# Optimization experiments

Hardware: AMD Instinct MI355X
Metric: run time of the kernel (lower is better)

Reference implementation:

```python
import jax, jax.numpy as jnp
import numpy as np

NG, NP = 4096, 512
ALPHA, BETA = 0.1, 0.5
NON_NEGATIVITY = True


def setup_inputs() -> dict:
    key = jax.random.key(0)
    k1, k2, k3, k4, k5 = jax.random.split(key, 5)
    B, T = 64, 100
    v = jax.random.normal(k1, (B, T, 2), dtype=jnp.float32)
    p0 = jax.random.normal(k2, (B, NP), dtype=jnp.float32)
    # xavier_uniform: limit = sqrt(6/(fan_in+fan_out))
    def xavier(k, shape):
        fan_out, fan_in = shape
        lim = float(np.sqrt(6.0 / (fan_in + fan_out)))
        return jax.random.uniform(k, shape, jnp.float32, -lim, lim)
    W_enc = xavier(k3, (NG, NP))   # init_position_encoder weight
    W_in = xavier(k4, (NG, 2))     # RNN weight_ih_l0
    W_h = xavier(k5, (NG, NG))     # RNN weight_hh_l0
    k6 = jax.random.fold_in(key, 6)
    W_dec = xavier(k6, (NP, NG))   # decoder weight
    return {"v": v, "p0": p0, "W_enc": W_enc, "W_in": W_in, "W_h": W_h, "W_dec": W_dec}


def _rnn(v, h0, W_in, W_h):
    # v: [B,T,2], h0: [B,Ng]
    def step(carry, v_t):
        hidden, vv, z_prev = carry
        z = v_t @ W_in.T + hidden @ W_h.T - BETA * vv  # [B,Ng]
        vv = vv + ALPHA * (z_prev - vv)
        if NON_NEGATIVITY:
            vv = jax.nn.relu(vv)
        s_z = jax.nn.relu(z)
        return (s_z, vv, z), s_z
    zeros = jnp.zeros_like(h0)
    _, out = jax.lax.scan(step, (h0, zeros, zeros), jnp.swapaxes(v, 0, 1))
    return jnp.swapaxes(out, 0, 1)  # [B,T,Ng]


def reference(v, p0, W_enc, W_in, W_h, W_dec):
    h0 = p0 @ W_enc.T                 # [B,Ng]
    gs = _rnn(v, h0, W_in, W_h)       # [B,T,Ng]
    logits = gs @ W_dec.T             # [B,T,Np]
    return jax.nn.log_softmax(logits, axis=-1)
```

## Files before the change

### kernel.cpp

```cpp
#include <hip/hip_runtime.h>
#include <hip/hip_bf16.h>

#define T_STEPS 100
#define NG 4096
#define NP 512

typedef __bf16 bf16x8 __attribute__((ext_vector_type(8)));
typedef float f32x4 __attribute__((ext_vector_type(4)));

__device__ __forceinline__ f32x4 mfma_bf16(bf16x8 a, bf16x8 b, f32x4 c) {
  return __builtin_amdgcn_mfma_f32_16x16x32_bf16(a, b, c, 0, 0, 0);
}

__device__ __forceinline__ void gload16(const void* g, void* l) {
  __builtin_amdgcn_global_load_lds(
      (const __attribute__((address_space(1))) void*)g,
      (__attribute__((address_space(3))) void*)l, 16, 0, 0);
}

__global__ __launch_bounds__(256) void cvt_bf16_kernel(const float* __restrict__ in,
                                                       __hip_bfloat16* __restrict__ out,
                                                       int n8) {
  int i = blockIdx.x * 256 + threadIdx.x;
  if (i >= n8) return;
  const float4* p = reinterpret_cast<const float4*>(in) + (size_t)i * 2;
  float4 f0 = p[0], f1 = p[1];
  union { __hip_bfloat16 h[8]; uint4 u; } z;
  z.h[0] = __float2bfloat16(f0.x); z.h[1] = __float2bfloat16(f0.y);
  z.h[2] = __float2bfloat16(f0.z); z.h[3] = __float2bfloat16(f0.w);
  z.h[4] = __float2bfloat16(f1.x); z.h[5] = __float2bfloat16(f1.y);
  z.h[6] = __float2bfloat16(f1.z); z.h[7] = __float2bfloat16(f1.w);
  *(reinterpret_cast<uint4*>(out) + i) = z.u;
}

__global__ __launch_bounds__(256) void encoder_kernel(const float* __restrict__ p0,
                                                      const float* __restrict__ Wenc,
                                                      __hip_bfloat16* __restrict__ h0) {
  __shared__ float sp[64 * 129];
  const int tid = threadIdx.x;
  const int nb = blockIdx.x * 16;
  const int b = tid & 63;
  const int jg = tid >> 6;
  float acc[4] = {0.f, 0.f, 0.f, 0.f};
  for (int kc = 0; kc < NP; kc += 128) {
    __syncthreads();
    #pragma unroll
    for (int i = 0; i < 32; ++i) {
      int e = tid + i * 256;
      int bb = e >> 7, kk = e & 127;
      sp[bb * 129 + kk] = p0[bb * NP + kc + kk];
    }
    __syncthreads();
    for (int kk = 0; kk < 128; ++kk) {
      float pv = sp[b * 129 + kk];
      #pragma unroll
      for (int jj = 0; jj < 4; ++jj)
        acc[jj] += pv * Wenc[(size_t)(nb + jg * 4 + jj) * NP + kc + kk];
    }
  }
  #pragma unroll
  for (int jj = 0; jj < 4; ++jj)
    h0[(size_t)b * NG + nb + jg * 4 + jj] = __float2bfloat16(acc[jj]);
}

__global__ __launch_bounds__(256, 2) void rnn_gemm_kernel(
    const __hip_bfloat16* __restrict__ A, int strideA,
    const __hip_bfloat16* __restrict__ Wh,
    float* __restrict__ zpart) {
  __shared__ char smem[65536];
  const int tid = threadIdx.x;
  const int lane = tid & 63;
  const int w = tid >> 6;
  const int ms = w >> 1, ns = w & 1;
  const int kq = blockIdx.x, ng = blockIdx.y;
  const int r = lane & 15;
  const int kg = lane >> 4;
  const int n0 = ng * 64;

  const __hip_bfloat16* gA = A + (size_t)kq * 512;
  const __hip_bfloat16* gB = Wh + (size_t)n0 * NG + (size_t)kq * 512;

  const int xsw = (kg ^ (r & 3)) << 4;
  const int xA0 = (ms * 32 + r) * 256 + xsw;
  const int xA1 = xA0 + 16 * 256;
  const int xB0 = (ns * 32 + r) * 256 + xsw;
  const int xB1 = xB0 + 16 * 256;
  const int x6 = (r & 4) << 4;
  const int ksX[4] = {0 ^ x6, 64 ^ x6, 128 ^ x6, 192 ^ x6};

  auto stageA = [&](int buf, int it) {
    #pragma unroll
    for (int i = 0; i < 4; ++i) {
      int c = i * 256 + tid;
      int row = c >> 4;
      int colB = (c & 15) * 16;
      int srcB = colB ^ ((row & 7) << 4);
      const char* src = (const char*)(gA + (size_t)row * strideA + it * 128) + srcB;
      gload16(src, smem + buf * 32768 + i * 4096 + w * 1024);
    }
  };
  auto stageB = [&](int buf, int it) {
    #pragma unroll
    for (int i = 0; i < 4; ++i) {
      int c = i * 256 + tid;
      int row = c >> 4;
      int colB = (c & 15) * 16;
      int srcB = colB ^ ((row & 7) << 4);
      const char* src = (const char*)(gB + (size_t)row * NG + it * 128) + srcB;
      gload16(src, smem + buf * 32768 + 16384 + i * 4096 + w * 1024);
    }
  };

  stageA(0, 0);
  stageB(0, 0);
  asm volatile("s_waitcnt vmcnt(0)" ::: "memory");
  __syncthreads();

  f32x4 acc00{}, acc01{}, acc10{}, acc11{};
  #pragma unroll
  for (int it = 0; it < 4; ++it) {
    const int buf = it & 1;
    if (it < 3) { stageA(buf ^ 1, it + 1); stageB(buf ^ 1, it + 1); }
    const char* bA = smem + buf * 32768;
    const char* bB = bA + 16384;
    #pragma unroll
    for (int ks = 0; ks < 4; ++ks) {
      bf16x8 a0 = *(const bf16x8*)(bA + xA0 + ksX[ks]);
      bf16x8 a1 = *(const bf16x8*)(bA + xA1 + ksX[ks]);
      bf16x8 b0 = *(const bf16x8*)(bB + xB0 + ksX[ks]);
      bf16x8 b1 = *(const bf16x8*)(bB + xB1 + ksX[ks]);
      acc00 = mfma_bf16(a0, b0, acc00);
      acc01 = mfma_bf16(a0, b1, acc01);
      acc10 = mfma_bf16(a1, b0, acc10);
      acc11 = mfma_bf16(a1, b1, acc11);
    }
    asm volatile("s_waitcnt vmcnt(0)" ::: "memory");
    __syncthreads();
  }

  float* zb = zpart + ((size_t)(kq * 64 + ms * 32 + kg * 4) << 12) + n0 + ns * 32 + r;
  #pragma unroll
  for (int j = 0; j < 4; ++j) {
    zb[(size_t)j * NG]             = acc00[j];
    zb[(size_t)j * NG + 16]        = acc01[j];
    zb[(size_t)(16 + j) * NG]      = acc10[j];
    zb[(size_t)(16 + j) * NG + 16] = acc11[j];
  }
}

__global__ __launch_bounds__(256) void rnn_epi_kernel(
    const float* __restrict__ zpart,
    const float* __restrict__ v, const float* __restrict__ Win,
    float* __restrict__ vv, float* __restrict__ zp,
    __hip_bfloat16* __restrict__ gs, int t) {
  const int g = blockIdx.x * 256 + threadIdx.x;
  const int b = g >> 10;
  const int n = (g & 1023) * 4;
  f32x4 s{};
  #pragma unroll
  for (int kq = 0; kq < 8; ++kq)
    s += *(const f32x4*)(zpart + ((size_t)(kq * 64 + b) << 12) + n);
  float2 vt = *(const float2*)(v + (b * T_STEPS + t) * 2);
  float4 wA = *(const float4*)(Win + 2 * n);
  float4 wB = *(const float4*)(Win + 2 * n + 4);
  f32x4 z;
  z[0] = s[0] + vt.x * wA.x + vt.y * wA.y;
  z[1] = s[1] + vt.x * wA.z + vt.y * wA.w;
  z[2] = s[2] + vt.x * wB.x + vt.y * wB.y;
  z[3] = s[3] + vt.x * wB.z + vt.y * wB.w;
  f32x4 vvo = *(const f32x4*)(vv + (size_t)b * NG + n);
  f32x4 zpo = *(const f32x4*)(zp + (size_t)b * NG + n);
  union { __hip_bfloat16 h[4]; uint2 u2; } o;
  f32x4 vvn;
  #pragma unroll
  for (int j = 0; j < 4; ++j) {
    z[j] -= 0.5f * vvo[j];
    vvn[j] = fmaxf(vvo[j] + 0.1f * (zpo[j] - vvo[j]), 0.f);
    o.h[j] = __float2bfloat16(fmaxf(z[j], 0.f));
  }
  *(f32x4*)(vv + (size_t)b * NG + n) = vvn;
  *(f32x4*)(zp + (size_t)b * NG + n) = z;
  *(uint2*)(gs + (size_t)(b * T_STEPS + t) * NG + n) = o.u2;
}

__global__ __launch_bounds__(256, 4) void decoder_kernel(
    const __hip_bfloat16* __restrict__ gs,
    const __hip_bfloat16* __restrict__ Wd,
    float* __restrict__ out) {
  __shared__ char smem[40960];
  const int tid = threadIdx.x;
  const int lane = tid & 63;
  const int w = tid >> 6;
  const int bid = blockIdx.x;
  const int xcd = bid & 7;
  const int i6 = bid >> 3;
  const int mtile = xcd * 25 + (i6 % 25);
  const int ntile = i6 / 25;
  const int m0 = mtile * 32;
  const int n0 = ntile * 128;
  const int r = lane & 15;
  const int kg = lane >> 4;

  const __hip_bfloat16* gA = gs + (size_t)m0 * NG;
  const __hip_bfloat16* gB = Wd + (size_t)n0 * NG;

  const int xsw = (kg * 16) ^ ((r & 3) << 4);
  const int x6 = (r & 4) << 4;
  const int ksX[2] = {0 ^ x6, 64 ^ x6};
  const int xA0 = r * 128 + xsw;
  const int xA1 = xA0 + 16 * 128;
  const int xB0 = (w * 32 + r) * 128 + xsw;
  const int xB1 = xB0 + 16 * 128;

  auto stageA = [&](int buf, int it) {
    int row = tid >> 3;
    int colB = (tid & 7) * 16;
    int srcB = colB ^ ((row & 7) << 4);
    const char* src = (const char*)(gA + (size_t)row * NG + it * 64) + srcB;
    gload16(src, smem + buf * 20480 + w * 1024);
  };
  auto stageB = [&](int buf, int it) {
    #pragma unroll
    for (int i = 0; i < 4; ++i) {
      int c = i * 256 + tid;
      int row = c >> 3;
      int colB = (c & 7) * 16;
      int srcB = colB ^ ((row & 7) << 4);
      const char* src = (const char*)(gB + (size_t)row * NG + it * 64) + srcB;
      gload16(src, smem + buf * 20480 + 4096 + i * 4096 + w * 1024);
    }
  };

  stageA(0, 0);
  stageB(0, 0);
  asm volatile("s_waitcnt vmcnt(0)" ::: "memory");
  __syncthreads();

  f32x4 acc00{}, acc01{}, acc10{}, acc11{};
  #pragma unroll 2
  for (int it = 0; it < 64; ++it) {
    const int buf = it & 1;
    if (it < 63) { stageA(buf ^ 1, it + 1); stageB(buf ^ 1, it + 1); }
    const char* bA = smem + buf * 20480;
    const char* bB = bA + 4096;
    #pragma unroll
    for (int ks = 0; ks < 2; ++ks) {
      bf16x8 a0 = *(const bf16x8*)(bA + xA0 + ksX[ks]);
      bf16x8 a1 = *(const bf16x8*)(bA + xA1 + ksX[ks]);
      bf16x8 b0 = *(const bf16x8*)(bB + xB0 + ksX[ks]);
      bf16x8 b1 = *(const bf16x8*)(bB + xB1 + ksX[ks]);
      acc00 = mfma_bf16(a0, b0, acc00);
      acc01 = mfma_bf16(a0, b1, acc01);
      acc10 = mfma_bf16(a1, b0, acc10);
      acc11 = mfma_bf16(a1, b1, acc11);
    }
    asm volatile("s_waitcnt vmcnt(0)" ::: "memory");
    __syncthreads();
  }

  #pragma unroll
  for (int j = 0; j < 4; ++j) {
    float* po0 = out + (size_t)(m0 + kg * 4 + j) * NP + n0 + w * 32;
    float* po1 = out + (size_t)(m0 + 16 + kg * 4 + j) * NP + n0 + w * 32;
    po0[r]      = acc00[j];
    po0[r + 16] = acc01[j];
    po1[r]      = acc10[j];
    po1[r + 16] = acc11[j];
  }
}

__global__ __launch_bounds__(256) void logsoftmax_kernel(float* __restrict__ out) {
  float* row = out + (size_t)blockIdx.x * NP;
  const int tid = threadIdx.x;
  const int lane = tid & 63, wid = tid >> 6;
  float x0 = row[tid], x1 = row[tid + 256];
  float m = fmaxf(x0, x1);
  #pragma unroll
  for (int off = 32; off >= 1; off >>= 1) m = fmaxf(m, __shfl_xor(m, off));
  __shared__ float sred[8];
  if (lane == 0) sred[wid] = m;
  __syncthreads();
  m = fmaxf(fmaxf(sred[0], sred[1]), fmaxf(sred[2], sred[3]));
  float e = __expf(x0 - m) + __expf(x1 - m);
  #pragma unroll
  for (int off = 32; off >= 1; off >>= 1) e += __shfl_xor(e, off);
  if (lane == 0) sred[4 + wid] = e;
  __syncthreads();
  float lse = m + __logf(sred[4] + sred[5] + sred[6] + sred[7]);
  row[tid] = x0 - lse;
  row[tid + 256] = x1 - lse;
}

extern "C" void kernel_launch(void* const* d_in, const int* in_sizes, int n_in,
                              void* d_out, int out_size, void* d_ws, size_t ws_size,
                              hipStream_t stream) {
  const float* v    = (const float*)d_in[0];
  const float* p0   = (const float*)d_in[1];
  const float* Wenc = (const float*)d_in[2];
  const float* Win  = (const float*)d_in[3];
  const float* Wh   = (const float*)d_in[4];
  const float* Wdec = (const float*)d_in[5];
  float* out = (float*)d_out;

  char* ws = (char*)d_ws;
  __hip_bfloat16* gs      = (__hip_bfloat16*)(ws);
  __hip_bfloat16* Wh_bf   = (__hip_bfloat16*)(ws + 52428800);
  float*          zpart   = (float*)(ws + 85983232);
  __hip_bfloat16* Wdec_bf = (__hip_bfloat16*)(ws + 85983232);
  float*          vv      = (float*)(ws + 94371840);
  float*          zp      = (float*)(ws + 95420416);
  __hip_bfloat16* h0_bf   = (__hip_bfloat16*)(ws + 96468992);

  hipMemsetAsync(vv, 0, 2 * 1048576, stream);
  cvt_bf16_kernel<<<8192, 256, 0, stream>>>(Wh, Wh_bf, 2097152);
  encoder_kernel<<<256, 256, 0, stream>>>(p0, Wenc, h0_bf);

  for (int t = 0; t < T_STEPS; ++t) {
    const __hip_bfloat16* A = (t == 0) ? h0_bf : (gs + (size_t)(t - 1) * NG);
    int sA = (t == 0) ? NG : T_STEPS * NG;
    rnn_gemm_kernel<<<dim3(8, 64), 256, 0, stream>>>(A, sA, Wh_bf, zpart);
    rnn_epi_kernel<<<256, 256, 0, stream>>>(zpart, v, Win, vv, zp, gs, t);
  }

  cvt_bf16_kernel<<<1024, 256, 0, stream>>>(Wdec, Wdec_bf, 262144);
  decoder_kernel<<<800, 256, 0, stream>>>(gs, Wdec_bf, out);
  logsoftmax_kernel<<<6400, 256, 0, stream>>>(out);
}
```

Before: 1.254 ms.

## Use triple-buffered 64-wide K tiles with single barrier per iteration in RNN GEMM

```diff
diff --git a/kernel.cpp b/kernel.cpp
--- a/kernel.cpp
+++ b/kernel.cpp
@@ -63,11 +63,11 @@
     h0[(size_t)b * NG + nb + jg * 4 + jj] = __float2bfloat16(acc[jj]);
 }
 
-__global__ __launch_bounds__(256, 2) void rnn_gemm_kernel(
+__global__ __launch_bounds__(256, 3) void rnn_gemm_kernel(
     const __hip_bfloat16* __restrict__ A, int strideA,
     const __hip_bfloat16* __restrict__ Wh,
     float* __restrict__ zpart) {
-  __shared__ char smem[65536];
+  __shared__ char smem[49152];
   const int tid = threadIdx.x;
   const int lane = tid & 63;
   const int w = tid >> 6;
@@ -81,61 +81,59 @@
   const __hip_bfloat16* gB = Wh + (size_t)n0 * NG + (size_t)kq * 512;
 
   const int xsw = (kg ^ (r & 3)) << 4;
-  const int xA0 = (ms * 32 + r) * 256 + xsw;
-  const int xA1 = xA0 + 16 * 256;
-  const int xB0 = (ns * 32 + r) * 256 + xsw;
-  const int xB1 = xB0 + 16 * 256;
   const int x6 = (r & 4) << 4;
-  const int ksX[4] = {0 ^ x6, 64 ^ x6, 128 ^ x6, 192 ^ x6};
+  const int ksX[2] = {0 ^ x6, 64 ^ x6};
+  const int xA0 = (ms * 32 + r) * 128 + xsw;
+  const int xA1 = xA0 + 16 * 128;
+  const int xB0 = 8192 + (ns * 32 + r) * 128 + xsw;
+  const int xB1 = xB0 + 16 * 128;
 
   auto stageA = [&](int buf, int it) {
     #pragma unroll
-    for (int i = 0; i < 4; ++i) {
+    for (int i = 0; i < 2; ++i) {
       int c = i * 256 + tid;
-      int row = c >> 4;
-      int colB = (c & 15) * 16;
+      int row = c >> 3;
+      int colB = (c & 7) * 16;
       int srcB = colB ^ ((row & 7) << 4);
-      const char* src = (const char*)(gA + (size_t)row * strideA + it * 128) + srcB;
-      gload16(src, smem + buf * 32768 + i * 4096 + w * 1024);
+      const char* src = (const char*)(gA + (size_t)row * strideA + it * 64) + srcB;
+      gload16(src, smem + buf * 16384 + i * 4096 + w * 1024);
     }
   };
   auto stageB = [&](int buf, int it) {
     #pragma unroll
-    for (int i = 0; i < 4; ++i) {
+    for (int i = 0; i < 2; ++i) {
       int c = i * 256 + tid;
-      int row = c >> 4;
-      int colB = (c & 15) * 16;
+      int row = c >> 3;
+      int colB = (c & 7) * 16;
       int srcB = colB ^ ((row & 7) << 4);
-      const char* src = (const char*)(gB + (size_t)row * NG + it * 128) + srcB;
-      gload16(src, smem + buf * 32768 + 16384 + i * 4096 + w * 1024);
+      const char* src = (const char*)(gB + (size_t)row * NG + it * 64) + srcB;
+      gload16(src, smem + buf * 16384 + 8192 + i * 4096 + w * 1024);
     }
   };
 
-  stageA(0, 0);
-  stageB(0, 0);
-  asm volatile("s_waitcnt vmcnt(0)" ::: "memory");
-  __syncthreads();
+  stageA(0, 0); stageB(0, 0);
+  stageA(1, 1); stageB(1, 1);
 
   f32x4 acc00{}, acc01{}, acc10{}, acc11{};
   #pragma unroll
-  for (int it = 0; it < 4; ++it) {
-    const int buf = it & 1;
-    if (it < 3) { stageA(buf ^ 1, it + 1); stageB(buf ^ 1, it + 1); }
-    const char* bA = smem + buf * 32768;
-    const char* bB = bA + 16384;
-    #pragma unroll
-    for (int ks = 0; ks < 4; ++ks) {
-      bf16x8 a0 = *(const bf16x8*)(bA + xA0 + ksX[ks]);
-      bf16x8 a1 = *(const bf16x8*)(bA + xA1 + ksX[ks]);
-      bf16x8 b0 = *(const bf16x8*)(bB + xB0 + ksX[ks]);
-      bf16x8 b1 = *(const bf16x8*)(bB + xB1 + ksX[ks]);
+  for (int it = 0; it < 8; ++it) {
+    if (it == 7) asm volatile("s_waitcnt vmcnt(0)" ::: "memory");
+    else         asm volatile("s_waitcnt vmcnt(4)" ::: "memory");
+    __builtin_amdgcn_s_barrier();
+    __builtin_amdgcn_sched_barrier(0);
+    if (it < 6) { stageA((it + 2) % 3, it + 2); stageB((it + 2) % 3, it + 2); }
+    const char* bb = smem + (it % 3) * 16384;
+    #pragma unroll
+    for (int ks = 0; ks < 2; ++ks) {
+      bf16x8 a0 = *(const bf16x8*)(bb + xA0 + ksX[ks]);
+      bf16x8 a1 = *(const bf16x8*)(bb + xA1 + ksX[ks]);
+      bf16x8 b0 = *(const bf16x8*)(bb + xB0 + ksX[ks]);
+      bf16x8 b1 = *(const bf16x8*)(bb + xB1 + ksX[ks]);
       acc00 = mfma_bf16(a0, b0, acc00);
       acc01 = mfma_bf16(a0, b1, acc01);
       acc10 = mfma_bf16(a1, b0, acc10);
       acc11 = mfma_bf16(a1, b1, acc11);
     }
-    asm volatile("s_waitcnt vmcnt(0)" ::: "memory");
-    __syncthreads();
   }
 
   float* zb = zpart + ((size_t)(kq * 64 + ms * 32 + kg * 4) << 12) + n0 + ns * 32 + r;
```

New measurement: 1.235 ms. No clear change (-1.5%).
